# Kernel tuning notes

Hardware: AMD Instinct MI355X
Metric: run time of the kernel (lower is better)

## Reference

```python
import jax, jax.numpy as jnp
import numpy as np

B, C, IN, OUT = 2048, 64, 512, 512


def setup_inputs() -> dict:
    key = jax.random.key(0)
    k1, k2, k3 = jax.random.split(key, 3)
    x = jax.random.normal(k1, (B, IN), dtype=jnp.float32)
    index = jax.random.randint(k2, (B,), 0, C, dtype=jnp.int64)
    # kaiming_uniform-ish init: bound = sqrt(6 / ((1 + 5) * fan_in)) = 1/sqrt(fan_in)
    bound = 1.0 / np.sqrt(IN)
    weight = jax.random.uniform(k3, (C, OUT, IN), dtype=jnp.float32,
                                minval=-bound, maxval=bound)
    return {"input": x, "index": index, "weight": weight}


def reference(input, index, weight):
    # weight: (C, OUT, IN); index: (B,); input: (B, IN)
    w = weight[index]                      # (B, OUT, IN) gathered per-sample matrix
    return jnp.einsum('boi,bi->bo', w, input)  # batched matvec -> (B, OUT)
```

## Files before the change

### kernel.cpp

```cpp
#include <hip/hip_runtime.h>


constexpr int Bsz  = 2048;
constexpr int Ccnt = 64;
constexpr int INF  = 512;
constexpr int OUTF = 512;
constexpr int THREADS = 256;
constexpr int OT = 32;
constexpr int NT = 64;
constexpr int NBLK = Ccnt * (OUTF / OT);

typedef __attribute__((ext_vector_type(8))) short bf16x8;
typedef __attribute__((ext_vector_type(4))) float f32x4;

#if __has_builtin(__builtin_amdgcn_cvt_pk_bf16_f32)
typedef __attribute__((ext_vector_type(2))) __bf16 bf16x2_t;
__device__ __forceinline__ int cvt2i(float a, float b) {
    union { bf16x2_t v; int i; } u;
    u.v = __builtin_amdgcn_cvt_pk_bf16_f32(a, b);
    return u.i;
}
#else
__device__ __forceinline__ unsigned f2bf(float f) {
    union { float f; unsigned u; } v; v.f = f;
    return (v.u + 0x7FFFu + ((v.u >> 16) & 1u)) >> 16;
}
__device__ __forceinline__ int cvt2i(float a, float b) {
    return (int)(f2bf(a) | (f2bf(b) << 16));
}
#endif

__device__ __forceinline__ bf16x8 cvt8(float4 a, float4 b) {
    union { bf16x8 v; int i[4]; } u;
    u.i[0] = cvt2i(a.x, a.y);
    u.i[1] = cvt2i(a.z, a.w);
    u.i[2] = cvt2i(b.x, b.y);
    u.i[3] = cvt2i(b.z, b.w);
    return u.v;
}

__global__ __launch_bounds__(THREADS, 4)
void switching_linear_kernel(const float* __restrict__ x,
                             const int* __restrict__ idx,
                             const float* __restrict__ w,
                             float* __restrict__ out) {
    __shared__ unsigned short list[Bsz];
    __shared__ int ls_n;
    __shared__ float red[2][16][64];

    const int tid = threadIdx.x;
    const int c  = blockIdx.x >> 4;
    const int o0 = (blockIdx.x & 15) * OT;

    if (tid == 0) ls_n = 0;
    __syncthreads();
    for (int i = tid; i < Bsz; i += THREADS) {
        if (idx[i] == c) list[atomicAdd(&ls_n, 1)] = (unsigned short)i;
    }
    __syncthreads();
    const int n = ls_n;
    if (n == 0) return;

    const int wave = tid >> 6;
    const int lane = tid & 63;
    const int r    = wave & 1;
    const int kh   = wave >> 1;
    const int mrow = lane & 15;
    const int quad = lane >> 4;
    const int ow   = o0 + r * 16;
    const int k0   = kh * (INF / 2);

    const float* aptr = w + ((size_t)c * OUTF + (size_t)(ow + mrow)) * INF
                          + k0 + quad * 8;

    for (int s0 = 0; s0 < n; s0 += NT) {
        const int rem = n - s0;
        const int ng  = rem >= NT ? 4 : (rem + 15) >> 4;

        const float* bptr[4];
        bool bval[4];
#pragma unroll
        for (int g = 0; g < 4; ++g) {
            int s = s0 + g * 16 + mrow;
            bval[g] = (s < n);
            int b = bval[g] ? (int)list[s] : 0;
            bptr[g] = x + (size_t)b * INF + k0 + quad * 8;
        }

        f32x4 acc[4] = {{0.f,0.f,0.f,0.f},{0.f,0.f,0.f,0.f},
                        {0.f,0.f,0.f,0.f},{0.f,0.f,0.f,0.f}};

#pragma unroll 4
        for (int kt = 0; kt < INF / 2; kt += 32) {
            float4 a0 = *(const float4*)(aptr + kt);
            float4 a1 = *(const float4*)(aptr + kt + 4);
            bf16x8 af = cvt8(a0, a1);

            for (int g = 0; g < ng; ++g) {
                bf16x8 bfr = {0,0,0,0,0,0,0,0};
                if (bval[g]) {
                    float4 b0 = *(const float4*)(bptr[g] + kt);
                    float4 b1 = *(const float4*)(bptr[g] + kt + 4);
                    bfr = cvt8(b0, b1);
                }
                acc[g] = __builtin_amdgcn_mfma_f32_16x16x32_bf16(af, bfr, acc[g], 0, 0, 0);
            }
        }

        if (kh == 1) {
#pragma unroll
            for (int g = 0; g < 4; ++g) {
                if (g < ng) {
#pragma unroll
                    for (int j = 0; j < 4; ++j) red[r][g * 4 + j][lane] = acc[g][j];
                }
            }
        }
        __syncthreads();
        if (kh == 0) {
#pragma unroll
            for (int g = 0; g < 4; ++g) {
                if (g < ng) {
                    int s = s0 + g * 16 + mrow;
                    if (s < n) {
                        float4 v;
                        v.x = acc[g][0] + red[r][g * 4 + 0][lane];
                        v.y = acc[g][1] + red[r][g * 4 + 1][lane];
                        v.z = acc[g][2] + red[r][g * 4 + 2][lane];
                        v.w = acc[g][3] + red[r][g * 4 + 3][lane];
                        float* dst = out + (size_t)list[s] * OUTF + ow + quad * 4;
                        *(float4*)dst = v;
                    }
                }
            }
        }
        __syncthreads();
    }
}

extern "C" void kernel_launch(void* const* d_in, const int* in_sizes, int n_in,
                              void* d_out, int out_size, void* d_ws, size_t ws_size,
                              hipStream_t stream) {
    const float* x   = (const float*)d_in[0];
    const int*   idx = (const int*)d_in[1];
    const float* w   = (const float*)d_in[2];
    float* out = (float*)d_out;

    switching_linear_kernel<<<dim3(NBLK), dim3(THREADS), 0, stream>>>(x, idx, w, out);
}
```

Measured before the change: 121.7 us.

## Stage weight tile in LDS via async global_load_lds, split samples across waves

The 32x512 weight slice is loaded into shared memory with direct global-to-LDS loads in MFMA fragment order, overlapped with the index scan. Each wave then handles its own 16-sample group over the full K range, so the cross-wave K-split reduction and its barriers are gone. Weights are read from LDS instead of repeatedly from global, but the 64KB LDS footprint drops occupancy (launch bounds 4 to 2), and per-wave sample partitioning leaves waves idle when a class has few samples.

```diff
diff --git a/kernel.cpp b/kernel.cpp
--- a/kernel.cpp
+++ b/kernel.cpp
@@ -39,102 +39,92 @@
     return u.v;
 }
 
-__global__ __launch_bounds__(THREADS, 4)
+__device__ __forceinline__ void gld_lds16(const float* g, float* l) {
+    __builtin_amdgcn_global_load_lds(
+        (const __attribute__((address_space(1))) float*)g,
+        (__attribute__((address_space(3))) float*)l, 16, 0, 0);
+}
+
+__global__ __launch_bounds__(THREADS, 2)
 void switching_linear_kernel(const float* __restrict__ x,
                              const int* __restrict__ idx,
                              const float* __restrict__ w,
                              float* __restrict__ out) {
+    __shared__ float Wl[OT * INF];
     __shared__ unsigned short list[Bsz];
     __shared__ int ls_n;
-    __shared__ float red[2][16][64];
 
-    const int tid = threadIdx.x;
+    const int tid  = threadIdx.x;
+    const int wave = tid >> 6;
+    const int lane = tid & 63;
     const int c  = blockIdx.x >> 4;
     const int o0 = (blockIdx.x & 15) * OT;
 
     if (tid == 0) ls_n = 0;
     __syncthreads();
-    for (int i = tid; i < Bsz; i += THREADS) {
-        if (idx[i] == c) list[atomicAdd(&ls_n, 1)] = (unsigned short)i;
+
+    int myidx[8];
+#pragma unroll
+    for (int i = 0; i < 8; ++i) myidx[i] = idx[tid + i * THREADS];
+
+    const float* wc = w + (size_t)c * OUTF * INF + (size_t)o0 * INF;
+#pragma unroll
+    for (int i = 0; i < 16; ++i) {
+        const int inst = wave * 16 + i;
+        const int ci = inst >> 1;
+        const int h  = inst & 1;
+        const int p  = h * 64 + lane;
+        const int l  = p >> 1;
+        const int row = (ci >> 4) * 16 + (l & 15);
+        const int gk  = 2 * (l >> 4) + (p & 1);
+        const float* src = wc + (size_t)row * INF + (ci & 15) * 32 + gk * 4;
+        gld_lds16(src, &Wl[ci * 512 + h * 256]);
     }
+
+#pragma unroll
+    for (int i = 0; i < 8; ++i) {
+        if (myidx[i] == c) list[atomicAdd(&ls_n, 1)] = (unsigned short)(tid + i * THREADS);
+    }
+
     __syncthreads();
     const int n = ls_n;
-    if (n == 0) return;
 
-    const int wave = tid >> 6;
-    const int lane = tid & 63;
-    const int r    = wave & 1;
-    const int kh   = wave >> 1;
     const int mrow = lane & 15;
     const int quad = lane >> 4;
-    const int ow   = o0 + r * 16;
-    const int k0   = kh * (INF / 2);
-
-    const float* aptr = w + ((size_t)c * OUTF + (size_t)(ow + mrow)) * INF
-                          + k0 + quad * 8;
+    const int lofs = lane * 8;
 
     for (int s0 = 0; s0 < n; s0 += NT) {
-        const int rem = n - s0;
-        const int ng  = rem >= NT ? 4 : (rem + 15) >> 4;
+        if (s0 + wave * 16 >= n) break;
+        const int s = s0 + wave * 16 + mrow;
+        const bool v = (s < n);
+        const float* bp = x + (size_t)(v ? (int)list[s] : 0) * INF + quad * 8;
 
-        const float* bptr[4];
-        bool bval[4];
-#pragma unroll
-        for (int g = 0; g < 4; ++g) {
-            int s = s0 + g * 16 + mrow;
-            bval[g] = (s < n);
-            int b = bval[g] ? (int)list[s] : 0;
-            bptr[g] = x + (size_t)b * INF + k0 + quad * 8;
+        f32x4 acc0 = {0.f,0.f,0.f,0.f}, acc1 = {0.f,0.f,0.f,0.f};
+
+#pragma unroll 4
+        for (int kt32 = 0; kt32 < 16; ++kt32) {
+            const float* ch0 = &Wl[kt32 * 512 + lofs];
+            const float* ch1 = &Wl[(16 + kt32) * 512 + lofs];
+            float4 a00 = *(const float4*)ch0;
+            float4 a01 = *(const float4*)(ch0 + 4);
+            float4 a10 = *(const float4*)ch1;
+            float4 a11 = *(const float4*)(ch1 + 4);
+
+            bf16x8 bfr = {0,0,0,0,0,0,0,0};
+            if (v) {
+                float4 b0 = *(const float4*)(bp + kt32 * 32);
+                float4 b1 = *(const float4*)(bp + kt32 * 32 + 4);
+                bfr = cvt8(b0, b1);
+            }
+            acc0 = __builtin_amdgcn_mfma_f32_16x16x32_bf16(cvt8(a00, a01), bfr, acc0, 0, 0, 0);
+            acc1 = __builtin_amdgcn_mfma_f32_16x16x32_bf16(cvt8(a10, a11), bfr, acc1, 0, 0, 0);
         }
 
-        f32x4 acc[4] = {{0.f,0.f,0.f,0.f},{0.f,0.f,0.f,0.f},
-                        {0.f,0.f,0.f,0.f},{0.f,0.f,0.f,0.f}};
-
-#pragma unroll 4
-        for (int kt = 0; kt < INF / 2; kt += 32) {
-            float4 a0 = *(const float4*)(aptr + kt);
-            float4 a1 = *(const float4*)(aptr + kt + 4);
-            bf16x8 af = cvt8(a0, a1);
-
-            for (int g = 0; g < ng; ++g) {
-                bf16x8 bfr = {0,0,0,0,0,0,0,0};
-                if (bval[g]) {
-                    float4 b0 = *(const float4*)(bptr[g] + kt);
-                    float4 b1 = *(const float4*)(bptr[g] + kt + 4);
-                    bfr = cvt8(b0, b1);
-                }
-                acc[g] = __builtin_amdgcn_mfma_f32_16x16x32_bf16(af, bfr, acc[g], 0, 0, 0);
-            }
+        if (v) {
+            float* d0 = out + (size_t)list[s] * OUTF + o0 + quad * 4;
+            *(float4*)d0 = make_float4(acc0[0], acc0[1], acc0[2], acc0[3]);
+            *(float4*)(d0 + 16) = make_float4(acc1[0], acc1[1], acc1[2], acc1[3]);
         }
-
-        if (kh == 1) {
-#pragma unroll
-            for (int g = 0; g < 4; ++g) {
-                if (g < ng) {
-#pragma unroll
-                    for (int j = 0; j < 4; ++j) red[r][g * 4 + j][lane] = acc[g][j];
-                }
-            }
-        }
-        __syncthreads();
-        if (kh == 0) {
-#pragma unroll
-            for (int g = 0; g < 4; ++g) {
-                if (g < ng) {
-                    int s = s0 + g * 16 + mrow;
-                    if (s < n) {
-                        float4 v;
-                        v.x = acc[g][0] + red[r][g * 4 + 0][lane];
-                        v.y = acc[g][1] + red[r][g * 4 + 1][lane];
-                        v.z = acc[g][2] + red[r][g * 4 + 2][lane];
-                        v.w = acc[g][3] + red[r][g * 4 + 3][lane];
-                        float* dst = out + (size_t)list[s] * OUTF + ow + quad * 4;
-                        *(float4*)dst = v;
-                    }
-                }
-            }
-        }
-        __syncthreads();
     }
 }
 
```

Result: faster. 116.5 us (-4.3%).

## Hold weight tile in registers with 4-way K split and 16-row output tiles

Applied to the files above, without the earlier changes.

Shrinks the output tile to 16 rows per block, which doubles the grid to 2048 blocks. Each of the four waves now owns a quarter of K, and its weight fragment is loaded into registers once, before the index scan finishes, so the weight fetch overlaps the list build. Each sample group's x values are loaded as a 4-wide K batch and fed to back-to-back MFMAs, and a three-way shared-memory reduction combines the K partials. This aims to raise occupancy and memory parallelism and to hide weight latency, at the cost of twice as many index scans and more x rereads across blocks.

```diff
diff --git a/kernel.cpp b/kernel.cpp
--- a/kernel.cpp
+++ b/kernel.cpp
@@ -6,8 +6,7 @@
 constexpr int INF  = 512;
 constexpr int OUTF = 512;
 constexpr int THREADS = 256;
-constexpr int OT = 32;
-constexpr int NT = 64;
+constexpr int OT = 16;
 constexpr int NBLK = Ccnt * (OUTF / OT);
 
 typedef __attribute__((ext_vector_type(8))) short bf16x8;
@@ -39,97 +38,102 @@
     return u.v;
 }
 
-__global__ __launch_bounds__(THREADS, 4)
+__global__ __launch_bounds__(THREADS, 3)
 void switching_linear_kernel(const float* __restrict__ x,
                              const int* __restrict__ idx,
                              const float* __restrict__ w,
                              float* __restrict__ out) {
     __shared__ unsigned short list[Bsz];
     __shared__ int ls_n;
-    __shared__ float red[2][16][64];
+    __shared__ float red[4][3][4][64];
 
-    const int tid = threadIdx.x;
-    const int c  = blockIdx.x >> 4;
-    const int o0 = (blockIdx.x & 15) * OT;
+    const int tid  = threadIdx.x;
+    const int wave = tid >> 6;
+    const int lane = tid & 63;
+    const int c  = blockIdx.x >> 5;
+    const int o0 = (blockIdx.x & 31) * OT;
+    const int mrow = lane & 15;
+    const int quad = lane >> 4;
+    const int k0   = wave * (INF / 4);
 
     if (tid == 0) ls_n = 0;
     __syncthreads();
-    for (int i = tid; i < Bsz; i += THREADS) {
-        if (idx[i] == c) list[atomicAdd(&ls_n, 1)] = (unsigned short)i;
-    }
+
+    int my[8];
+#pragma unroll
+    for (int i = 0; i < 8; ++i) my[i] = idx[tid + i * THREADS];
+
+    const float* aptr = w + ((size_t)c * OUTF + (size_t)(o0 + mrow)) * INF
+                          + k0 + quad * 8;
+    float4 wv[8];
+#pragma unroll
+    for (int i = 0; i < 8; ++i)
+        wv[i] = *(const float4*)(aptr + (i >> 1) * 32 + (i & 1) * 4);
+
+#pragma unroll
+    for (int i = 0; i < 8; ++i)
+        if (my[i] == c) list[atomicAdd(&ls_n, 1)] = (unsigned short)(tid + i * THREADS);
+
     __syncthreads();
     const int n = ls_n;
-    if (n == 0) return;
 
-    const int wave = tid >> 6;
-    const int lane = tid & 63;
-    const int r    = wave & 1;
-    const int kh   = wave >> 1;
-    const int mrow = lane & 15;
-    const int quad = lane >> 4;
-    const int ow   = o0 + r * 16;
-    const int k0   = kh * (INF / 2);
+    bf16x8 wf[4];
+#pragma unroll
+    for (int i = 0; i < 4; ++i) wf[i] = cvt8(wv[2 * i], wv[2 * i + 1]);
 
-    const float* aptr = w + ((size_t)c * OUTF + (size_t)(ow + mrow)) * INF
-                          + k0 + quad * 8;
+    for (int s0 = 0; s0 < n; s0 += 64) {
+        const int rem = n - s0;
+        const int ng  = rem >= 64 ? 4 : (rem + 15) >> 4;
 
-    for (int s0 = 0; s0 < n; s0 += NT) {
-        const int rem = n - s0;
-        const int ng  = rem >= NT ? 4 : (rem + 15) >> 4;
+        f32x4 acc[4];
+#pragma unroll
+        for (int g = 0; g < 4; ++g) acc[g] = (f32x4){0.f, 0.f, 0.f, 0.f};
 
-        const float* bptr[4];
-        bool bval[4];
+#pragma unroll 2
+        for (int g = 0; g < ng; ++g) {
+            const int s = s0 + g * 16 + mrow;
+            const bool v = (s < n);
+            const float* bp = x + (size_t)(v ? (int)list[s] : 0) * INF + k0 + quad * 8;
+            bf16x8 xf[4];
+            if (v) {
 #pragma unroll
-        for (int g = 0; g < 4; ++g) {
-            int s = s0 + g * 16 + mrow;
-            bval[g] = (s < n);
-            int b = bval[g] ? (int)list[s] : 0;
-            bptr[g] = x + (size_t)b * INF + k0 + quad * 8;
+                for (int i = 0; i < 4; ++i) {
+                    float4 b0 = *(const float4*)(bp + i * 32);
+                    float4 b1 = *(const float4*)(bp + i * 32 + 4);
+                    xf[i] = cvt8(b0, b1);
+                }
+            } else {
+#pragma unroll
+                for (int i = 0; i < 4; ++i) xf[i] = (bf16x8){0,0,0,0,0,0,0,0};
+            }
+#pragma unroll
+            for (int i = 0; i < 4; ++i)
+                acc[g] = __builtin_amdgcn_mfma_f32_16x16x32_bf16(wf[i], xf[i], acc[g], 0, 0, 0);
         }
 
-        f32x4 acc[4] = {{0.f,0.f,0.f,0.f},{0.f,0.f,0.f,0.f},
-                        {0.f,0.f,0.f,0.f},{0.f,0.f,0.f,0.f}};
-
-#pragma unroll 4
-        for (int kt = 0; kt < INF / 2; kt += 32) {
-            float4 a0 = *(const float4*)(aptr + kt);
-            float4 a1 = *(const float4*)(aptr + kt + 4);
-            bf16x8 af = cvt8(a0, a1);
-
-            for (int g = 0; g < ng; ++g) {
-                bf16x8 bfr = {0,0,0,0,0,0,0,0};
-                if (bval[g]) {
-                    float4 b0 = *(const float4*)(bptr[g] + kt);
-                    float4 b1 = *(const float4*)(bptr[g] + kt + 4);
-                    bfr = cvt8(b0, b1);
-                }
-                acc[g] = __builtin_amdgcn_mfma_f32_16x16x32_bf16(af, bfr, acc[g], 0, 0, 0);
-            }
-        }
-
-        if (kh == 1) {
+        if (wave != 0) {
 #pragma unroll
             for (int g = 0; g < 4; ++g) {
                 if (g < ng) {
 #pragma unroll
-                    for (int j = 0; j < 4; ++j) red[r][g * 4 + j][lane] = acc[g][j];
+                    for (int j = 0; j < 4; ++j) red[g][wave - 1][j][lane] = acc[g][j];
                 }
             }
         }
         __syncthreads();
-        if (kh == 0) {
+        if (wave == 0) {
 #pragma unroll
             for (int g = 0; g < 4; ++g) {
                 if (g < ng) {
-                    int s = s0 + g * 16 + mrow;
+                    const int s = s0 + g * 16 + mrow;
                     if (s < n) {
-                        float4 v;
-                        v.x = acc[g][0] + red[r][g * 4 + 0][lane];
-                        v.y = acc[g][1] + red[r][g * 4 + 1][lane];
-                        v.z = acc[g][2] + red[r][g * 4 + 2][lane];
-                        v.w = acc[g][3] + red[r][g * 4 + 3][lane];
-                        float* dst = out + (size_t)list[s] * OUTF + ow + quad * 4;
-                        *(float4*)dst = v;
+                        f32x4 a = acc[g];
+#pragma unroll
+                        for (int wv2 = 0; wv2 < 3; ++wv2)
+#pragma unroll
+                            for (int j = 0; j < 4; ++j) a[j] += red[g][wv2][j][lane];
+                        float* dst = out + (size_t)list[s] * OUTF + o0 + quad * 4;
+                        *(float4*)dst = make_float4(a[0], a[1], a[2], a[3]);
                     }
                 }
             }
```

New measurement: 113.3 us. 1.07x faster.
